# Optimization experiments

Hardware: AMD Instinct MI355X
Metric: run time of the kernel (lower is better)

## Reference

```python
import jax, jax.numpy as jnp
import numpy as np

N_NODES = 10000
N_EDGES = 640000
N_GRAPHS = 64
IN_FEATS = 128
H_FEATS = 128


def setup_inputs() -> dict:
    key = jax.random.key(0)
    ks = jax.random.split(key, 8)
    in_feat = jax.random.normal(ks[0], (N_NODES, IN_FEATS), dtype=jnp.float32)
    src = jax.random.randint(ks[1], (N_EDGES,), 0, N_NODES, dtype=jnp.int32)
    dst = jax.random.randint(ks[2], (N_EDGES,), 0, N_NODES, dtype=jnp.int32)
    graph_ids = jnp.sort(jax.random.randint(ks[3], (N_NODES,), 0, N_GRAPHS, dtype=jnp.int32))
    s1 = 1.0 / np.sqrt(IN_FEATS)
    s2 = 1.0 / np.sqrt(H_FEATS)
    W1 = jax.random.uniform(ks[4], (IN_FEATS, H_FEATS), jnp.float32, -s1, s1)
    b1 = jnp.zeros((H_FEATS,), jnp.float32)
    W2 = jax.random.uniform(ks[5], (H_FEATS, H_FEATS), jnp.float32, -s2, s2)
    b2 = jnp.zeros((H_FEATS,), jnp.float32)
    Wd = jax.random.uniform(ks[6], (H_FEATS, 1), jnp.float32, -s2, s2)
    bd = jnp.zeros((1,), jnp.float32)
    return {"in_feat": in_feat, "src": src, "dst": dst, "graph_ids": graph_ids,
            "W1": W1, "b1": b1, "W2": W2, "b2": b2, "Wd": Wd, "bd": bd}


def _graph_conv(x, src, dst, norm_src, norm_dst, W, b):
    # DGL GraphConv, norm='both': D_dst^{-1/2} A D_src^{-1/2} X W + b
    x = x * norm_src[:, None]
    agg = jax.ops.segment_sum(x[src], dst, num_segments=N_NODES)  # scatter-add over edges
    agg = agg * norm_dst[:, None]
    return agg @ W + b


def reference(in_feat, src, dst, graph_ids, W1, b1, W2, b2, Wd, bd):
    ones_e = jnp.ones((N_EDGES,), in_feat.dtype)
    out_deg = jax.ops.segment_sum(ones_e, src, num_segments=N_NODES)
    in_deg = jax.ops.segment_sum(ones_e, dst, num_segments=N_NODES)
    norm_src = jnp.where(out_deg > 0, out_deg, 1.0) ** -0.5
    norm_dst = jnp.where(in_deg > 0, in_deg, 1.0) ** -0.5

    h = jax.nn.relu(_graph_conv(in_feat, src, dst, norm_src, norm_dst, W1, b1))
    h = jax.nn.relu(_graph_conv(h, src, dst, norm_src, norm_dst, W2, b2))

    # dgl.mean_nodes: per-graph mean of node features
    counts = jax.ops.segment_sum(jnp.ones((N_NODES,), h.dtype), graph_ids, num_segments=N_GRAPHS)
    pooled = jax.ops.segment_sum(h, graph_ids, num_segments=N_GRAPHS)
    pooled = pooled / jnp.maximum(counts, 1.0)[:, None]

    out = pooled @ Wd + bd  # [G, 1]
    return out.squeeze(-1)
```

## Files before the change

### kernel.cpp

```cpp
#include <hip/hip_runtime.h>
#include <hip/hip_fp16.h>

#define N_NODES 10000
#define N_EDGES 640000
#define N_GRAPHS 64
#define FEATS 128

#define NSLICE 64
#define EPS (N_EDGES / NSLICE)
#define CAP 160

static inline size_t align_up(size_t x, size_t a) { return (x + a - 1) & ~(a - 1); }

__global__ __launch_bounds__(256) void hist_kernel(const int* __restrict__ src,
                                                   const int* __restrict__ dst,
                                                   int* __restrict__ counts,
                                                   int* __restrict__ scounts) {
    __shared__ int h[N_NODES];
    const int tid = threadIdx.x;
    const int b = blockIdx.x;
    const bool is_dst = (b < NSLICE);
    const int slice = is_dst ? b : b - NSLICE;
    const int* col = is_dst ? dst : src;
    int* outp = (is_dst ? counts : scounts) + slice * N_NODES;

    for (int i = tid; i < N_NODES; i += 256) h[i] = 0;
    __syncthreads();
    const int4* c4 = (const int4*)(col + slice * EPS);
    for (int i = tid; i < EPS / 4; i += 256) {
        int4 v = c4[i];
        atomicAdd(&h[v.x], 1);
        atomicAdd(&h[v.y], 1);
        atomicAdd(&h[v.z], 1);
        atomicAdd(&h[v.w], 1);
    }
    __syncthreads();
    for (int i = tid; i < N_NODES; i += 256) outp[i] = h[i];
}

__global__ __launch_bounds__(256) void degnorm_base_kernel(int* __restrict__ counts,
                                                           const int* __restrict__ scounts,
                                                           const int* __restrict__ gids,
                                                           int* __restrict__ deg_in,
                                                           float* __restrict__ norm_src,
                                                           float* __restrict__ norm_dst,
                                                           int* __restrict__ graph_cnt) {
    __shared__ int gcnt[N_GRAPHS];
    const int tid = threadIdx.x;
    if (tid < N_GRAPHS) gcnt[tid] = 0;
    __syncthreads();
    int n = blockIdx.x * 256 + tid;
    if (n < N_NODES) {
        int run = n * CAP;
        for (int s = 0; s < NSLICE; s++) {
            int c = counts[s * N_NODES + n];
            counts[s * N_NODES + n] = run;
            run += c;
        }
        int di = run - n * CAP;
        int dou = 0;
        for (int s = 0; s < NSLICE; s++) dou += scounts[s * N_NODES + n];
        deg_in[n] = di;
        norm_dst[n] = rsqrtf((float)(di < 1 ? 1 : di));
        norm_src[n] = rsqrtf((float)(dou < 1 ? 1 : dou));
        atomicAdd(&gcnt[gids[n]], 1);
    }
    __syncthreads();
    if (tid < N_GRAPHS && gcnt[tid]) atomicAdd(&graph_cnt[tid], gcnt[tid]);
}

__global__ __launch_bounds__(256) void scatter_kernel(const int* __restrict__ src,
                                                      const int* __restrict__ dst,
                                                      const int* __restrict__ base,
                                                      int* __restrict__ sorted_src) {
    __shared__ int cur[N_NODES];
    const int tid = threadIdx.x;
    const int s = blockIdx.x;
    for (int i = tid; i < N_NODES; i += 256) cur[i] = base[s * N_NODES + i];
    __syncthreads();
    const int4* s4 = (const int4*)(src + s * EPS);
    const int4* d4 = (const int4*)(dst + s * EPS);
    for (int i = tid; i < EPS / 4; i += 256) {
        int4 sv = s4[i];
        int4 dv = d4[i];
        int p;
        p = atomicAdd(&cur[dv.x], 1); sorted_src[p] = sv.x;
        p = atomicAdd(&cur[dv.y], 1); sorted_src[p] = sv.y;
        p = atomicAdd(&cur[dv.z], 1); sorted_src[p] = sv.z;
        p = atomicAdd(&cur[dv.w], 1); sorted_src[p] = sv.w;
    }
}

__global__ __launch_bounds__(256) void prescale_kernel(const float* __restrict__ in_feat,
                                                       const float* __restrict__ norm_src,
                                                       __half* __restrict__ xs) {
    int i = blockIdx.x * 256 + threadIdx.x;
    if (i < N_NODES * (FEATS / 4)) {
        int n = i >> 5;
        float4 v = ((const float4*)in_feat)[i];
        float s = norm_src[n];
        __half2 h0 = __floats2half2_rn(v.x * s, v.y * s);
        __half2 h1 = __floats2half2_rn(v.z * s, v.w * s);
        __half2* o = (__half2*)(xs + (size_t)i * 4);
        o[0] = h0; o[1] = h1;
    }
}

__global__ __launch_bounds__(256) void aggregate_kernel(const __half* __restrict__ X,
                                                        const int* __restrict__ sorted_src,
                                                        const int* __restrict__ deg_in,
                                                        const float* __restrict__ norm_dst,
                                                        float* __restrict__ out) {
    const int tid = threadIdx.x;
    const int wave = tid >> 6, lane = tid & 63;
    const int grp = lane >> 4, l16 = lane & 15;
    const int n = blockIdx.x * 4 + wave;
    const int start = n * CAP;
    const int cnt = deg_in[n];
    const uint4* __restrict__ x4 = (const uint4*)X;
    float acc[8] = {0.f, 0.f, 0.f, 0.f, 0.f, 0.f, 0.f, 0.f};

    int c = grp;
    for (; c + 12 < cnt; c += 16) {
        int idx[4];
#pragma unroll
        for (int k = 0; k < 4; k++) idx[k] = sorted_src[start + c + 4 * k];
        uint4 v[4];
#pragma unroll
        for (int k = 0; k < 4; k++) v[k] = x4[idx[k] * 16 + l16];
#pragma unroll
        for (int k = 0; k < 4; k++) {
            const __half2* hp = (const __half2*)&v[k];
#pragma unroll
            for (int j = 0; j < 4; j++) {
                float2 f = __half22float2(hp[j]);
                acc[2 * j]     += f.x;
                acc[2 * j + 1] += f.y;
            }
        }
    }
    for (; c < cnt; c += 4) {
        uint4 v = x4[sorted_src[start + c] * 16 + l16];
        const __half2* hp = (const __half2*)&v;
#pragma unroll
        for (int j = 0; j < 4; j++) {
            float2 f = __half22float2(hp[j]);
            acc[2 * j]     += f.x;
            acc[2 * j + 1] += f.y;
        }
    }
#pragma unroll
    for (int j = 0; j < 8; j++) {
        acc[j] += __shfl_xor(acc[j], 16);
        acc[j] += __shfl_xor(acc[j], 32);
    }
    if (grp == 0) {
        const float nd = norm_dst[n];
        float4 o0 = make_float4(acc[0] * nd, acc[1] * nd, acc[2] * nd, acc[3] * nd);
        float4 o1 = make_float4(acc[4] * nd, acc[5] * nd, acc[6] * nd, acc[7] * nd);
        float4* op = (float4*)(out + (size_t)n * FEATS + l16 * 8);
        op[0] = o0; op[1] = o1;
    }
}

__global__ __launch_bounds__(256) void gemm_relu_scale_kernel(const float* __restrict__ A,
                                                              const float* __restrict__ W,
                                                              const float* __restrict__ bias,
                                                              const float* __restrict__ scale,
                                                              __half* __restrict__ out) {
    __shared__ float As[16 * FEATS];
    int tid = threadIdx.x;
    int nb = blockIdx.x * 16;
    const float4* av = (const float4*)(A + (size_t)nb * FEATS);
    float4* sv = (float4*)As;
    sv[tid]       = av[tid];
    sv[tid + 256] = av[tid + 256];
    __syncthreads();
    int fg = (tid & 31) << 2;
    int r  = tid >> 5;
    const float* a0p = As + r * FEATS;
    const float* a1p = As + (r + 8) * FEATS;
    float4 acc0 = make_float4(0.f, 0.f, 0.f, 0.f);
    float4 acc1 = make_float4(0.f, 0.f, 0.f, 0.f);
#pragma unroll 4
    for (int k = 0; k < FEATS; k++) {
        float a0 = a0p[k];
        float a1 = a1p[k];
        float4 w = *(const float4*)(W + k * FEATS + fg);
        acc0.x = fmaf(a0, w.x, acc0.x); acc0.y = fmaf(a0, w.y, acc0.y);
        acc0.z = fmaf(a0, w.z, acc0.z); acc0.w = fmaf(a0, w.w, acc0.w);
        acc1.x = fmaf(a1, w.x, acc1.x); acc1.y = fmaf(a1, w.y, acc1.y);
        acc1.z = fmaf(a1, w.z, acc1.z); acc1.w = fmaf(a1, w.w, acc1.w);
    }
    float4 bb = *(const float4*)(bias + fg);
    int gn0 = nb + r, gn1 = nb + r + 8;
    float s0 = scale[gn0], s1 = scale[gn1];
    __half2 h00 = __floats2half2_rn(fmaxf(acc0.x + bb.x, 0.f) * s0,
                                    fmaxf(acc0.y + bb.y, 0.f) * s0);
    __half2 h01 = __floats2half2_rn(fmaxf(acc0.z + bb.z, 0.f) * s0,
                                    fmaxf(acc0.w + bb.w, 0.f) * s0);
    __half2 h10 = __floats2half2_rn(fmaxf(acc1.x + bb.x, 0.f) * s1,
                                    fmaxf(acc1.y + bb.y, 0.f) * s1);
    __half2 h11 = __floats2half2_rn(fmaxf(acc1.z + bb.z, 0.f) * s1,
                                    fmaxf(acc1.w + bb.w, 0.f) * s1);
    __half2* o0 = (__half2*)(out + (size_t)gn0 * FEATS + fg);
    __half2* o1 = (__half2*)(out + (size_t)gn1 * FEATS + fg);
    o0[0] = h00; o0[1] = h01;
    o1[0] = h10; o1[1] = h11;
}

__global__ __launch_bounds__(256) void gemm_relu_pool_kernel(const float* __restrict__ A,
                                                             const float* __restrict__ W,
                                                             const float* __restrict__ bias,
                                                             const float* __restrict__ Wd,
                                                             const int* __restrict__ gids,
                                                             float* __restrict__ graph_sum) {
    __shared__ float As[16 * FEATS];
    __shared__ float bins[N_GRAPHS];
    int tid = threadIdx.x;
    int nb = blockIdx.x * 16;
    const float4* av = (const float4*)(A + (size_t)nb * FEATS);
    float4* sv = (float4*)As;
    sv[tid]       = av[tid];
    sv[tid + 256] = av[tid + 256];
    if (tid < N_GRAPHS) bins[tid] = 0.f;
    __syncthreads();
    int fg = (tid & 31) << 2;
    int r  = tid >> 5;
    const float* a0p = As + r * FEATS;
    const float* a1p = As + (r + 8) * FEATS;
    float4 acc0 = make_float4(0.f, 0.f, 0.f, 0.f);
    float4 acc1 = make_float4(0.f, 0.f, 0.f, 0.f);
#pragma unroll 4
    for (int k = 0; k < FEATS; k++) {
        float a0 = a0p[k];
        float a1 = a1p[k];
        float4 w = *(const float4*)(W + k * FEATS + fg);
        acc0.x = fmaf(a0, w.x, acc0.x); acc0.y = fmaf(a0, w.y, acc0.y);
        acc0.z = fmaf(a0, w.z, acc0.z); acc0.w = fmaf(a0, w.w, acc0.w);
        acc1.x = fmaf(a1, w.x, acc1.x); acc1.y = fmaf(a1, w.y, acc1.y);
        acc1.z = fmaf(a1, w.z, acc1.z); acc1.w = fmaf(a1, w.w, acc1.w);
    }
    float4 bb = *(const float4*)(bias + fg);
    float4 wd = *(const float4*)(Wd + fg);
    float p0 = fmaxf(acc0.x + bb.x, 0.f) * wd.x + fmaxf(acc0.y + bb.y, 0.f) * wd.y +
               fmaxf(acc0.z + bb.z, 0.f) * wd.z + fmaxf(acc0.w + bb.w, 0.f) * wd.w;
    float p1 = fmaxf(acc1.x + bb.x, 0.f) * wd.x + fmaxf(acc1.y + bb.y, 0.f) * wd.y +
               fmaxf(acc1.z + bb.z, 0.f) * wd.z + fmaxf(acc1.w + bb.w, 0.f) * wd.w;
#pragma unroll
    for (int d = 16; d >= 1; d >>= 1) {
        p0 += __shfl_down(p0, d);
        p1 += __shfl_down(p1, d);
    }
    if ((tid & 31) == 0) {
        int gn0 = nb + r, gn1 = nb + r + 8;
        atomicAdd(&bins[gids[gn0]], p0);
        atomicAdd(&bins[gids[gn1]], p1);
    }
    __syncthreads();
    if (tid < N_GRAPHS) {
        float v = bins[tid];
        if (v != 0.f) atomicAdd(&graph_sum[tid], v);
    }
}

__global__ __launch_bounds__(64) void final_kernel(const float* __restrict__ graph_sum,
                                                   const int* __restrict__ graph_cnt,
                                                   const float* __restrict__ bd,
                                                   float* __restrict__ out) {
    int g = threadIdx.x;
    if (g < N_GRAPHS) {
        out[g] = graph_sum[g] / fmaxf((float)graph_cnt[g], 1.f) + bd[0];
    }
}

extern "C" void kernel_launch(void* const* d_in, const int* in_sizes, int n_in,
                              void* d_out, int out_size, void* d_ws, size_t ws_size,
                              hipStream_t stream) {
    const float* in_feat = (const float*)d_in[0];
    const int*   src     = (const int*)d_in[1];
    const int*   dst     = (const int*)d_in[2];
    const int*   gids    = (const int*)d_in[3];
    const float* W1      = (const float*)d_in[4];
    const float* b1      = (const float*)d_in[5];
    const float* W2      = (const float*)d_in[6];
    const float* b2      = (const float*)d_in[7];
    const float* Wd      = (const float*)d_in[8];
    const float* bd      = (const float*)d_in[9];
    float* out = (float*)d_out;

    char* ws = (char*)d_ws;
    size_t off = 0;
    int* graph_cnt = (int*)(ws + off); off += N_GRAPHS * 4;
    float* graph_sum = (float*)(ws + off); off += N_GRAPHS * 4;
    size_t zero_bytes = off;
    off = align_up(off, 512);
    int* counts  = (int*)(ws + off); off += (size_t)NSLICE * N_NODES * 4;
    off = align_up(off, 512);
    int* scounts = (int*)(ws + off); off += (size_t)NSLICE * N_NODES * 4;
    off = align_up(off, 512);
    int* deg_in  = (int*)(ws + off); off += N_NODES * 4;
    off = align_up(off, 512);
    float* norm_src = (float*)(ws + off); off += N_NODES * 4;
    off = align_up(off, 512);
    float* norm_dst = (float*)(ws + off); off += N_NODES * 4;
    off = align_up(off, 512);
    int* sorted_src = (int*)(ws + off); off += (size_t)N_NODES * CAP * 4 + 4096;
    off = align_up(off, 512);
    __half* xs  = (__half*)(ws + off); off += (size_t)N_NODES * FEATS * 2;
    off = align_up(off, 512);
    __half* h   = (__half*)(ws + off); off += (size_t)N_NODES * FEATS * 2;
    off = align_up(off, 512);
    float* agg1 = (float*)(ws + off); off += (size_t)N_NODES * FEATS * 4;
    off = align_up(off, 512);
    float* agg2 = (float*)(ws + off); off += (size_t)N_NODES * FEATS * 4;
    (void)ws_size;

    hipMemsetAsync(ws, 0, zero_bytes, stream);

    hist_kernel<<<2 * NSLICE, 256, 0, stream>>>(src, dst, counts, scounts);
    degnorm_base_kernel<<<(N_NODES + 255) / 256, 256, 0, stream>>>(counts, scounts, gids,
                                                                   deg_in, norm_src, norm_dst,
                                                                   graph_cnt);
    scatter_kernel<<<NSLICE, 256, 0, stream>>>(src, dst, counts, sorted_src);
    prescale_kernel<<<(N_NODES * (FEATS / 4) + 255) / 256, 256, 0, stream>>>(in_feat,
                                                                             norm_src, xs);

    aggregate_kernel<<<N_NODES / 4, 256, 0, stream>>>(xs, sorted_src, deg_in, norm_dst, agg1);
    gemm_relu_scale_kernel<<<N_NODES / 16, 256, 0, stream>>>(agg1, W1, b1, norm_src, h);

    aggregate_kernel<<<N_NODES / 4, 256, 0, stream>>>(h, sorted_src, deg_in, norm_dst, agg2);
    gemm_relu_pool_kernel<<<N_NODES / 16, 256, 0, stream>>>(agg2, W2, b2, Wd, gids,
                                                            graph_sum);

    final_kernel<<<1, 64, 0, stream>>>(graph_sum, graph_cnt, bd, out);
}
```

Measured before the change: 175.3 us.

## Fuse aggregation into GEMM kernels, prescale into degnorm, and final into pool

Gathers each 16-node tile directly into shared memory inside the layer GEMM kernels, so the fp32 agg1/agg2 buffers are never written to or read back from global memory. The feature prescale moves into the degree-normalisation kernel, and the final division runs in whichever block finishes last, tracked by an atomic done counter. This drops three launches and two large intermediate round-trips. The cost is a different gather mapping: each 16-lane group now walks one node's whole edge list alone, with 8-way unrolling instead of four groups sharing a node, which may hurt load balance and memory parallelism.

```diff
diff --git a/kernel.cpp b/kernel.cpp
--- a/kernel.cpp
+++ b/kernel.cpp
@@ -9,6 +9,7 @@
 #define NSLICE 64
 #define EPS (N_EDGES / NSLICE)
 #define CAP 160
+#define NBLK (N_NODES / 16)
 
 static inline size_t align_up(size_t x, size_t a) { return (x + a - 1) & ~(a - 1); }
 
@@ -41,15 +42,20 @@
 __global__ __launch_bounds__(256) void degnorm_base_kernel(int* __restrict__ counts,
                                                            const int* __restrict__ scounts,
                                                            const int* __restrict__ gids,
+                                                           const float* __restrict__ in_feat,
                                                            int* __restrict__ deg_in,
                                                            float* __restrict__ norm_src,
                                                            float* __restrict__ norm_dst,
-                                                           int* __restrict__ graph_cnt) {
+                                                           int* __restrict__ graph_cnt,
+                                                           __half* __restrict__ xs) {
     __shared__ int gcnt[N_GRAPHS];
-    const int tid = threadIdx.x;
+    __shared__ float ns_l[256];
+    const int tid = threadIdx.x;
+    const int base_n = blockIdx.x * 256;
     if (tid < N_GRAPHS) gcnt[tid] = 0;
     __syncthreads();
-    int n = blockIdx.x * 256 + tid;
+    int n = base_n + tid;
+    float ns = 0.f;
     if (n < N_NODES) {
         int run = n * CAP;
         for (int s = 0; s < NSLICE; s++) {
@@ -62,11 +68,27 @@
         for (int s = 0; s < NSLICE; s++) dou += scounts[s * N_NODES + n];
         deg_in[n] = di;
         norm_dst[n] = rsqrtf((float)(di < 1 ? 1 : di));
-        norm_src[n] = rsqrtf((float)(dou < 1 ? 1 : dou));
+        ns = rsqrtf((float)(dou < 1 ? 1 : dou));
+        norm_src[n] = ns;
         atomicAdd(&gcnt[gids[n]], 1);
     }
+    ns_l[tid] = ns;
     __syncthreads();
     if (tid < N_GRAPHS && gcnt[tid]) atomicAdd(&graph_cnt[tid], gcnt[tid]);
+
+    const float4* inf4 = (const float4*)in_feat;
+    for (int i = tid; i < 256 * 32; i += 256) {
+        int nloc = i >> 5;
+        int n2 = base_n + nloc;
+        if (n2 < N_NODES) {
+            float4 v = inf4[(size_t)n2 * 32 + (i & 31)];
+            float s = ns_l[nloc];
+            __half2 h0 = __floats2half2_rn(v.x * s, v.y * s);
+            __half2 h1 = __floats2half2_rn(v.z * s, v.w * s);
+            __half2* o = (__half2*)(xs + (size_t)n2 * FEATS + (i & 31) * 4);
+            o[0] = h0; o[1] = h1;
+        }
+    }
 }
 
 __global__ __launch_bounds__(256) void scatter_kernel(const int* __restrict__ src,
@@ -91,45 +113,30 @@
     }
 }
 
-__global__ __launch_bounds__(256) void prescale_kernel(const float* __restrict__ in_feat,
-                                                       const float* __restrict__ norm_src,
-                                                       __half* __restrict__ xs) {
-    int i = blockIdx.x * 256 + threadIdx.x;
-    if (i < N_NODES * (FEATS / 4)) {
-        int n = i >> 5;
-        float4 v = ((const float4*)in_feat)[i];
-        float s = norm_src[n];
-        __half2 h0 = __floats2half2_rn(v.x * s, v.y * s);
-        __half2 h1 = __floats2half2_rn(v.z * s, v.w * s);
-        __half2* o = (__half2*)(xs + (size_t)i * 4);
-        o[0] = h0; o[1] = h1;
-    }
-}
-
-__global__ __launch_bounds__(256) void aggregate_kernel(const __half* __restrict__ X,
-                                                        const int* __restrict__ sorted_src,
-                                                        const int* __restrict__ deg_in,
-                                                        const float* __restrict__ norm_dst,
-                                                        float* __restrict__ out) {
-    const int tid = threadIdx.x;
+__device__ __forceinline__ void gather16(const __half* __restrict__ X,
+                                         const int* __restrict__ sorted_src,
+                                         const int* __restrict__ deg_in,
+                                         const float* __restrict__ norm_dst,
+                                         int nb, int tid, float* As) {
     const int wave = tid >> 6, lane = tid & 63;
     const int grp = lane >> 4, l16 = lane & 15;
-    const int n = blockIdx.x * 4 + wave;
+    const int nloc = wave * 4 + grp;
+    const int n = nb + nloc;
     const int start = n * CAP;
     const int cnt = deg_in[n];
     const uint4* __restrict__ x4 = (const uint4*)X;
     float acc[8] = {0.f, 0.f, 0.f, 0.f, 0.f, 0.f, 0.f, 0.f};
 
-    int c = grp;
-    for (; c + 12 < cnt; c += 16) {
-        int idx[4];
-#pragma unroll
-        for (int k = 0; k < 4; k++) idx[k] = sorted_src[start + c + 4 * k];
-        uint4 v[4];
-#pragma unroll
-        for (int k = 0; k < 4; k++) v[k] = x4[idx[k] * 16 + l16];
-#pragma unroll
-        for (int k = 0; k < 4; k++) {
+    int c = 0;
+    for (; c + 8 <= cnt; c += 8) {
+        int idx[8];
+#pragma unroll
+        for (int k = 0; k < 8; k++) idx[k] = sorted_src[start + c + k];
+        uint4 v[8];
+#pragma unroll
+        for (int k = 0; k < 8; k++) v[k] = x4[idx[k] * 16 + l16];
+#pragma unroll
+        for (int k = 0; k < 8; k++) {
             const __half2* hp = (const __half2*)&v[k];
 #pragma unroll
             for (int j = 0; j < 4; j++) {
@@ -139,7 +146,7 @@
             }
         }
     }
-    for (; c < cnt; c += 4) {
+    for (; c < cnt; c++) {
         uint4 v = x4[sorted_src[start + c] * 16 + l16];
         const __half2* hp = (const __half2*)&v;
 #pragma unroll
@@ -149,33 +156,27 @@
             acc[2 * j + 1] += f.y;
         }
     }
-#pragma unroll
-    for (int j = 0; j < 8; j++) {
-        acc[j] += __shfl_xor(acc[j], 16);
-        acc[j] += __shfl_xor(acc[j], 32);
-    }
-    if (grp == 0) {
-        const float nd = norm_dst[n];
-        float4 o0 = make_float4(acc[0] * nd, acc[1] * nd, acc[2] * nd, acc[3] * nd);
-        float4 o1 = make_float4(acc[4] * nd, acc[5] * nd, acc[6] * nd, acc[7] * nd);
-        float4* op = (float4*)(out + (size_t)n * FEATS + l16 * 8);
-        op[0] = o0; op[1] = o1;
-    }
-}
-
-__global__ __launch_bounds__(256) void gemm_relu_scale_kernel(const float* __restrict__ A,
-                                                              const float* __restrict__ W,
-                                                              const float* __restrict__ bias,
-                                                              const float* __restrict__ scale,
-                                                              __half* __restrict__ out) {
+    const float nd = norm_dst[n];
+    float4 o0 = make_float4(acc[0] * nd, acc[1] * nd, acc[2] * nd, acc[3] * nd);
+    float4 o1 = make_float4(acc[4] * nd, acc[5] * nd, acc[6] * nd, acc[7] * nd);
+    float4* op = (float4*)(As + nloc * FEATS + l16 * 8);
+    op[0] = o0; op[1] = o1;
+}
+
+__global__ __launch_bounds__(256) void layer1_kernel(const __half* __restrict__ X,
+                                                     const int* __restrict__ sorted_src,
+                                                     const int* __restrict__ deg_in,
+                                                     const float* __restrict__ norm_dst,
+                                                     const float* __restrict__ W,
+                                                     const float* __restrict__ bias,
+                                                     const float* __restrict__ scale,
+                                                     __half* __restrict__ out) {
     __shared__ float As[16 * FEATS];
-    int tid = threadIdx.x;
-    int nb = blockIdx.x * 16;
-    const float4* av = (const float4*)(A + (size_t)nb * FEATS);
-    float4* sv = (float4*)As;
-    sv[tid]       = av[tid];
-    sv[tid + 256] = av[tid + 256];
-    __syncthreads();
+    const int tid = threadIdx.x;
+    const int nb = blockIdx.x * 16;
+    gather16(X, sorted_src, deg_in, norm_dst, nb, tid, As);
+    __syncthreads();
+
     int fg = (tid & 31) << 2;
     int r  = tid >> 5;
     const float* a0p = As + r * FEATS;
@@ -209,22 +210,28 @@
     o1[0] = h10; o1[1] = h11;
 }
 
-__global__ __launch_bounds__(256) void gemm_relu_pool_kernel(const float* __restrict__ A,
-                                                             const float* __restrict__ W,
-                                                             const float* __restrict__ bias,
-                                                             const float* __restrict__ Wd,
-                                                             const int* __restrict__ gids,
-                                                             float* __restrict__ graph_sum) {
+__global__ __launch_bounds__(256) void layer2_kernel(const __half* __restrict__ X,
+                                                     const int* __restrict__ sorted_src,
+                                                     const int* __restrict__ deg_in,
+                                                     const float* __restrict__ norm_dst,
+                                                     const float* __restrict__ W,
+                                                     const float* __restrict__ bias,
+                                                     const float* __restrict__ Wd,
+                                                     const int* __restrict__ gids,
+                                                     float* __restrict__ graph_sum,
+                                                     const int* __restrict__ graph_cnt,
+                                                     const float* __restrict__ bd,
+                                                     int* __restrict__ done_counter,
+                                                     float* __restrict__ out) {
     __shared__ float As[16 * FEATS];
     __shared__ float bins[N_GRAPHS];
-    int tid = threadIdx.x;
-    int nb = blockIdx.x * 16;
-    const float4* av = (const float4*)(A + (size_t)nb * FEATS);
-    float4* sv = (float4*)As;
-    sv[tid]       = av[tid];
-    sv[tid + 256] = av[tid + 256];
+    __shared__ int lastflag;
+    const int tid = threadIdx.x;
+    const int nb = blockIdx.x * 16;
     if (tid < N_GRAPHS) bins[tid] = 0.f;
-    __syncthreads();
+    gather16(X, sorted_src, deg_in, norm_dst, nb, tid, As);
+    __syncthreads();
+
     int fg = (tid & 31) << 2;
     int r  = tid >> 5;
     const float* a0p = As + r * FEATS;
@@ -262,15 +269,16 @@
         float v = bins[tid];
         if (v != 0.f) atomicAdd(&graph_sum[tid], v);
     }
-}
-
-__global__ __launch_bounds__(64) void final_kernel(const float* __restrict__ graph_sum,
-                                                   const int* __restrict__ graph_cnt,
-                                                   const float* __restrict__ bd,
-                                                   float* __restrict__ out) {
-    int g = threadIdx.x;
-    if (g < N_GRAPHS) {
-        out[g] = graph_sum[g] / fmaxf((float)graph_cnt[g], 1.f) + bd[0];
+    __threadfence();
+    __syncthreads();
+    if (tid == 0) {
+        int done = atomicAdd(done_counter, 1);
+        lastflag = (done == gridDim.x - 1);
+    }
+    __syncthreads();
+    if (lastflag && tid < N_GRAPHS) {
+        float v = atomicAdd(&graph_sum[tid], 0.f);
+        out[tid] = v / fmaxf((float)graph_cnt[tid], 1.f) + bd[0];
     }
 }
 
@@ -293,6 +301,7 @@
     size_t off = 0;
     int* graph_cnt = (int*)(ws + off); off += N_GRAPHS * 4;
     float* graph_sum = (float*)(ws + off); off += N_GRAPHS * 4;
+    int* done_counter = (int*)(ws + off); off += 64;
     size_t zero_bytes = off;
     off = align_up(off, 512);
     int* counts  = (int*)(ws + off); off += (size_t)NSLICE * N_NODES * 4;
@@ -307,31 +316,22 @@
     off = align_up(off, 512);
     int* sorted_src = (int*)(ws + off); off += (size_t)N_NODES * CAP * 4 + 4096;
     off = align_up(off, 512);
-    __half* xs  = (__half*)(ws + off); off += (size_t)N_NODES * FEATS * 2;
-    off = align_up(off, 512);
-    __half* h   = (__half*)(ws + off); off += (size_t)N_NODES * FEATS * 2;
-    off = align_up(off, 512);
-    float* agg1 = (float*)(ws + off); off += (size_t)N_NODES * FEATS * 4;
-    off = align_up(off, 512);
-    float* agg2 = (float*)(ws + off); off += (size_t)N_NODES * FEATS * 4;
+    __half* xs = (__half*)(ws + off); off += (size_t)N_NODES * FEATS * 2;
+    off = align_up(off, 512);
+    __half* h  = (__half*)(ws + off); off += (size_t)N_NODES * FEATS * 2;
     (void)ws_size;
 
     hipMemsetAsync(ws, 0, zero_bytes, stream);
 
     hist_kernel<<<2 * NSLICE, 256, 0, stream>>>(src, dst, counts, scounts);
     degnorm_base_kernel<<<(N_NODES + 255) / 256, 256, 0, stream>>>(counts, scounts, gids,
-                                                                   deg_in, norm_src, norm_dst,
-                                                                   graph_cnt);
+                                                                   in_feat, deg_in, norm_src,
+                                                                   norm_dst, graph_cnt, xs);
     scatter_kernel<<<NSLICE, 256, 0, stream>>>(src, dst, counts, sorted_src);
-    prescale_kernel<<<(N_NODES * (FEATS / 4) + 255) / 256, 256, 0, stream>>>(in_feat,
-                                                                             norm_src, xs);
-
-    aggregate_kernel<<<N_NODES / 4, 256, 0, stream>>>(xs, sorted_src, deg_in, norm_dst, agg1);
-    gemm_relu_scale_kernel<<<N_NODES / 16, 256, 0, stream>>>(agg1, W1, b1, norm_src, h);
-
-    aggregate_kernel<<<N_NODES / 4, 256, 0, stream>>>(h, sorted_src, deg_in, norm_dst, agg2);
-    gemm_relu_pool_kernel<<<N_NODES / 16, 256, 0, stream>>>(agg2, W2, b2, Wd, gids,
-                                                            graph_sum);
-
-    final_kernel<<<1, 64, 0, stream>>>(graph_sum, graph_cnt, bd, out);
-}
+
+    layer1_kernel<<<NBLK, 256, 0, stream>>>(xs, sorted_src, deg_in, norm_dst,
+                                            W1, b1, norm_src, h);
+    layer2_kernel<<<NBLK, 256, 0, stream>>>(h, sorted_src, deg_in, norm_dst,
+                                            W2, b2, Wd, gids, graph_sum, graph_cnt,
+                                            bd, done_counter, out);
+}
```

New measurement: 210.9 us. +20.3%, slower.
